# Performance work log

Measured on AMD Instinct MI355X. Metric: run time of the kernel, lower is better.

## Reference

```python
import jax, jax.numpy as jnp
import numpy as np

B, L, DIN, DM, NL = 2, 1024, 512, 1024, 4
E, N, R, K = 2048, 16, 64, 4  # d_inner, d_state, dt_rank, d_conv


def setup_inputs() -> dict:
    key = jax.random.key(0)
    ks = iter(jax.random.split(key, 32))
    rn = lambda sh, s=1.0: jax.random.normal(next(ks), sh, jnp.float32) * s
    A_init = jnp.broadcast_to(jnp.arange(1, N + 1, dtype=jnp.float32), (NL, E, N))
    return dict(
        x=rn((B, L, DIN)),
        z=rn((B, L, DIN)),
        ip_w=rn((DM, DIN), 0.02), ip_b=jnp.zeros((DM,), jnp.float32),
        ln_w=jnp.ones((NL, DM), jnp.float32), ln_b=jnp.zeros((NL, DM), jnp.float32),
        inproj_w=rn((NL, 2 * E, DM), 0.02),
        conv_w=rn((NL, E, K), 0.1), conv_b=jnp.zeros((NL, E), jnp.float32),
        xproj_w=rn((NL, R + 2 * N, E), 0.02),
        dtproj_w=rn((NL, E, R), 0.05), dtproj_b=rn((NL, E), 0.1),
        A_log=jnp.log(A_init),
        Dp=jnp.ones((NL, E), jnp.float32),
        outproj_w=rn((NL, DM, E), 0.02),
        fnorm_w=jnp.ones((DM,), jnp.float32), fnorm_b=jnp.zeros((DM,), jnp.float32),
        op_w=rn((DIN, DM), 0.02), op_b=jnp.zeros((DIN,), jnp.float32),
    )


def layernorm(x, w, b, eps=1e-5):
    m = x.mean(-1, keepdims=True)
    v = ((x - m) ** 2).mean(-1, keepdims=True)
    return (x - m) * jax.lax.rsqrt(v + eps) * w + b


def dwconv_causal(xm, w, b):
    # xm: (B, L, E); w: (E, K) depthwise kernel; causal left padding
    xc = xm.transpose(0, 2, 1)  # (B, E, L)
    out = jax.lax.conv_general_dilated(
        xc, w[:, None, :], (1,), [(K - 1, 0)],
        feature_group_count=E, dimension_numbers=('NCH', 'OIH', 'NCH'))
    return (out + b[:, None]).transpose(0, 2, 1)


def selective_scan(u, dt, A, Bm, Cm, D):
    # u, dt: (B, L, E); A: (E, N); Bm, Cm: (B, L, N); D: (E,)
    h0 = jnp.zeros((u.shape[0], E, N), u.dtype)

    def step(h, inp):
        dt_t, u_t, B_t, C_t = inp  # (B,E),(B,E),(B,N),(B,N)
        dA = jnp.exp(dt_t[..., None] * A)                      # (B, E, N)
        h = dA * h + (dt_t * u_t)[..., None] * B_t[:, None, :]  # (B, E, N)
        y = jnp.einsum('ben,bn->be', h, C_t)
        return h, y

    _, ys = jax.lax.scan(step, h0, (dt.transpose(1, 0, 2), u.transpose(1, 0, 2),
                                    Bm.transpose(1, 0, 2), Cm.transpose(1, 0, 2)))
    return ys.transpose(1, 0, 2) + u * D  # (B, L, E)


def mamba_block(x, inproj_w, conv_w, conv_b, xproj_w, dtproj_w, dtproj_b, A_log, Dp, outproj_w):
    xz = jnp.einsum('bld,ed->ble', x, inproj_w)  # (B, L, 2E)
    xm, zg = xz[..., :E], xz[..., E:]
    xm = jax.nn.silu(dwconv_causal(xm, conv_w, conv_b))
    x_dbl = jnp.einsum('ble,re->blr', xm, xproj_w)  # (B, L, R+2N)
    dt = jax.nn.softplus(jnp.einsum('blr,er->ble', x_dbl[..., :R], dtproj_w) + dtproj_b)
    Bm = x_dbl[..., R:R + N]
    Cm = x_dbl[..., R + N:]
    A = -jnp.exp(A_log)  # (E, N)
    y = selective_scan(xm, dt, A, Bm, Cm, Dp)
    y = y * jax.nn.silu(zg)
    return jnp.einsum('ble,de->bld', y, outproj_w)


def reference(x, z, ip_w, ip_b, ln_w, ln_b, inproj_w, conv_w, conv_b, xproj_w,
              dtproj_w, dtproj_b, A_log, Dp, outproj_w, fnorm_w, fnorm_b, op_w, op_b):
    # z is accepted but unused, matching the original forward(x, z)
    h = jnp.einsum('bld,hd->blh', x, ip_w) + ip_b
    for l in range(NL):
        hn = layernorm(h, ln_w[l], ln_b[l])
        h = h + mamba_block(hn, inproj_w[l], conv_w[l], conv_b[l], xproj_w[l],
                            dtproj_w[l], dtproj_b[l], A_log[l], Dp[l], outproj_w[l])
    h = layernorm(h, fnorm_w, fnorm_b)
    return jnp.einsum('blh,oh->blo', h, op_w) + op_b
```

## Files before the change

kernel.cpp:

```cpp
#include <hip/hip_runtime.h>
#include <math.h>

#define BB 2
#define LL 1024
#define DIN_ 512
#define DM_ 1024
#define NL_ 4
#define EE 2048
#define NN 16
#define RR 64
#define KK 4

#define NC 32
#define CT 32

typedef unsigned short ushort_t;
typedef unsigned int uint_t;

using frag_ab = __attribute__((ext_vector_type(8))) short;
using frag_cd = __attribute__((ext_vector_type(4))) float;

__device__ __forceinline__ float softplus_f(float x) {
    return fmaxf(x, 0.f) + log1pf(expf(-fabsf(x)));
}
__device__ __forceinline__ float silu_fast(float x) {
    return x / (1.f + __expf(-x));
}
__device__ __forceinline__ float bf2f(ushort_t x) {
    return __uint_as_float((uint_t)x << 16);
}
__device__ __forceinline__ ushort_t f2bf(float x) {
    uint_t u = __float_as_uint(x);
    uint_t r = (u + 0x7fffu + ((u >> 16) & 1u)) >> 16;
    return (ushort_t)r;
}
__device__ __forceinline__ void gload_lds16(const void* g, void* l) {
    __builtin_amdgcn_global_load_lds(
        (const __attribute__((address_space(1))) void*)g,
        (__attribute__((address_space(3))) void*)l, 16, 0, 0);
}

__global__ __launch_bounds__(256) void cvt_bf16_kernel(
    ushort_t* __restrict__ o, const float* __restrict__ in, int n4)
{
    int i = blockIdx.x * 256 + threadIdx.x;
    if (i >= n4) return;
    float4 v = ((const float4*)in)[i];
    ushort4 u;
    u.x = f2bf(v.x); u.y = f2bf(v.y); u.z = f2bf(v.z); u.w = f2bf(v.w);
    ((ushort4*)o)[i] = u;
}

template <int EPI, int NT, int OUTBF>
__global__ __launch_bounds__(256) void mgemm_kernel(
    void* __restrict__ Cp, const ushort_t* __restrict__ A,
    const ushort_t* __restrict__ W, const float* __restrict__ bias,
    int N, int K, int lda, int ldw, int ldc, int pstride)
{
    __shared__ __attribute__((aligned(16))) ushort_t As[2][8 * 512];
    __shared__ __attribute__((aligned(16))) ushort_t Bs[2][NT * 512];

    const int tid = threadIdx.x;
    const int w = tid >> 6;
    const int lane = tid & 63;
    const int r = lane & 15;
    const int q = lane >> 4;
    const int m0 = blockIdx.y * 128;
    const int n0 = blockIdx.x * (NT * 16);
    const int wm = w >> 1;
    const int wn = w & 1;
    const int NWT = NT / 2;

    frag_cd acc[4][NWT];
#pragma unroll
    for (int i = 0; i < 4; i++)
#pragma unroll
        for (int j = 0; j < NWT; j++)
#pragma unroll
            for (int t = 0; t < 4; t++) acc[i][j][t] = 0.f;

    size_t koff = (EPI == 5) ? (size_t)blockIdx.z * K : 0;
    const ushort_t* Ab = A + (size_t)m0 * lda + koff;
    const ushort_t* Wb = W + (size_t)n0 * ldw + koff;

    const int NFRAG = 8 + NT;
    auto stage = [&](int k0, int buf) {
        for (int F = w; F < NFRAG; F += 4) {
            if (F < 8) {
                gload_lds16(Ab + (size_t)(F * 16 + r) * lda + k0 + q * 8,
                            &As[buf][F * 512]);
            } else {
                int nt = F - 8;
                if (n0 + nt * 16 + r < N)
                    gload_lds16(Wb + (size_t)(nt * 16 + r) * ldw + k0 + q * 8,
                                &Bs[buf][nt * 512]);
            }
        }
    };

    stage(0, 0);
    int buf = 0;
    for (int k0 = 0; k0 < K; k0 += 32) {
        __syncthreads();
        if (k0 + 32 < K) stage(k0 + 32, buf ^ 1);
        frag_ab af[4], bf[NWT];
#pragma unroll
        for (int i = 0; i < 4; i++)
            af[i] = *(const frag_ab*)(&As[buf][(wm * 4 + i) * 512] + lane * 8);
#pragma unroll
        for (int j = 0; j < NWT; j++)
            bf[j] = *(const frag_ab*)(&Bs[buf][(wn * NWT + j) * 512] + lane * 8);
#pragma unroll
        for (int i = 0; i < 4; i++)
#pragma unroll
            for (int j = 0; j < NWT; j++)
                acc[i][j] = __builtin_amdgcn_mfma_f32_16x16x32_bf16(
                    af[i], bf[j], acc[i][j], 0, 0, 0);
        buf ^= 1;
    }

    float* Cf = (float*)Cp;
    ushort_t* Cb = (ushort_t*)Cp;
    float* Cpart = (EPI == 5) ? Cf + (size_t)blockIdx.z * pstride : Cf;
#pragma unroll
    for (int i = 0; i < 4; i++) {
        int mrow = m0 + (wm * 4 + i) * 16 + q * 4;
#pragma unroll
        for (int j = 0; j < NWT; j++) {
            int col = n0 + (wn * NWT + j) * 16 + r;
            if (col >= N) continue;
            float bv = (EPI == 2) ? bias[col] : 0.f;
#pragma unroll
            for (int t = 0; t < 4; t++) {
                float v = acc[i][j][t];
                size_t idx = (size_t)(mrow + t) * ldc + col;
                if (EPI == 5) { Cpart[idx] = v; continue; }
                if (EPI == 2) v = softplus_f(v + bv);
                if (OUTBF) Cb[idx] = f2bf(v);
                else       Cf[idx] = v;
            }
        }
    }
}

__global__ __launch_bounds__(256) void reduce_ln_kernel(
    float* __restrict__ h, ushort_t* __restrict__ hn,
    const float* __restrict__ parts, int nparts, int pstride4,
    const float* __restrict__ bias,
    const float* __restrict__ w, const float* __restrict__ b, int hasres)
{
    const int row = blockIdx.x;
    const int tid = threadIdx.x;
    const int i4 = row * (DM_ / 4) + tid;

    float4 v = make_float4(0.f, 0.f, 0.f, 0.f);
    if (hasres) v = ((const float4*)h)[i4];
    for (int p = 0; p < nparts; p++) {
        float4 t = ((const float4*)parts)[(size_t)p * pstride4 + i4];
        v.x += t.x; v.y += t.y; v.z += t.z; v.w += t.w;
    }
    if (bias) {
        float4 t = ((const float4*)bias)[tid];
        v.x += t.x; v.y += t.y; v.z += t.z; v.w += t.w;
    }
    ((float4*)h)[i4] = v;

    float s = v.x + v.y + v.z + v.w;
    float sq = v.x * v.x + v.y * v.y + v.z * v.z + v.w * v.w;
#pragma unroll
    for (int off = 32; off; off >>= 1) {
        s += __shfl_down(s, off);
        sq += __shfl_down(sq, off);
    }
    __shared__ float ls[4], lq[4];
    int wid = tid >> 6;
    if ((tid & 63) == 0) { ls[wid] = s; lq[wid] = sq; }
    __syncthreads();
    float S = ls[0] + ls[1] + ls[2] + ls[3];
    float Q = lq[0] + lq[1] + lq[2] + lq[3];
    float mean = S * (1.f / DM_);
    float var = Q * (1.f / DM_) - mean * mean;
    float inv = rsqrtf(var + 1e-5f);
    float4 wv = ((const float4*)w)[tid];
    float4 bv = ((const float4*)b)[tid];
    ushort4 o;
    o.x = f2bf((v.x - mean) * inv * wv.x + bv.x);
    o.y = f2bf((v.y - mean) * inv * wv.y + bv.y);
    o.z = f2bf((v.z - mean) * inv * wv.z + bv.z);
    o.w = f2bf((v.w - mean) * inv * wv.w + bv.w);
    ((ushort4*)hn)[i4] = o;
}

__global__ __launch_bounds__(256) void reduce_xdb_kernel(
    float* __restrict__ xdb, ushort_t* __restrict__ xdbb,
    const float* __restrict__ parts, int pstride4, int total4)
{
    int i = blockIdx.x * 256 + threadIdx.x;
    if (i >= total4) return;
    float4 v = make_float4(0.f, 0.f, 0.f, 0.f);
#pragma unroll
    for (int p = 0; p < 16; p++) {
        float4 t = ((const float4*)parts)[(size_t)p * pstride4 + i];
        v.x += t.x; v.y += t.y; v.z += t.z; v.w += t.w;
    }
    ((float4*)xdb)[i] = v;
    ushort4 u;
    u.x = f2bf(v.x); u.y = f2bf(v.y); u.z = f2bf(v.z); u.w = f2bf(v.w);
    ((ushort4*)xdbb)[i] = u;
}

__global__ __launch_bounds__(256) void reduce_bias_kernel(
    float* __restrict__ out, const float* __restrict__ parts,
    const float* __restrict__ bias, int pstride4, int n4, int total4)
{
    int i = blockIdx.x * 256 + threadIdx.x;
    if (i >= total4) return;
    float4 v = ((const float4*)bias)[i % n4];
#pragma unroll
    for (int p = 0; p < 4; p++) {
        float4 t = ((const float4*)parts)[(size_t)p * pstride4 + i];
        v.x += t.x; v.y += t.y; v.z += t.z; v.w += t.w;
    }
    ((float4*)out)[i] = v;
}

__global__ __launch_bounds__(256) void conv_silu_kernel(
    ushort_t* __restrict__ xm, const ushort_t* __restrict__ xz,
    const float* __restrict__ cw, const float* __restrict__ cb)
{
    const int e = blockIdx.x * 256 + threadIdx.x;
    const int t0 = blockIdx.y * 4;
    const int b = blockIdx.z;
    const ushort_t* X = xz + (size_t)b * LL * 2 * EE + e;
    float4 w4 = ((const float4*)cw)[e];
    float wk[4] = {w4.x, w4.y, w4.z, w4.w};
    float cbv = cb[e];
    float v[7];
#pragma unroll
    for (int k = 0; k < 7; k++) {
        int t = t0 - 3 + k;
        v[k] = (t >= 0) ? bf2f(X[(size_t)t * 2 * EE]) : 0.f;
    }
    ushort_t* Y = xm + ((size_t)b * LL + t0) * EE + e;
#pragma unroll
    for (int j = 0; j < 4; j++) {
        float acc = cbv;
#pragma unroll
        for (int k = 0; k < 4; k++) acc = fmaf(wk[k], v[j + k], acc);
        Y[(size_t)j * EE] = f2bf(silu_fast(acc));
    }
}

__global__ __launch_bounds__(256) void scan_phase1_kernel(
    float* __restrict__ Pg, float* __restrict__ Sg,
    const float* __restrict__ dt, const ushort_t* __restrict__ u,
    const float* __restrict__ xdb, const float* __restrict__ A_log)
{
    const int tid = threadIdx.x;
    const int e = blockIdx.x * 256 + tid;
    const int c = blockIdx.y;
    const int b = blockIdx.z;
    const int t0 = c * CT;

    __shared__ float Bs[CT][16];
    {
        int tt = tid >> 3;
        int jj = tid & 7;
        if (jj < 4) {
            float4 v = *(const float4*)(xdb + ((size_t)(b * LL + t0 + tt) * 96 + 64 + jj * 4));
            *(float4*)&Bs[tt][jj * 4] = v;
        }
    }
    __syncthreads();

    float Ae[16];
#pragma unroll
    for (int k = 0; k < 4; k++) {
        float4 a = *(const float4*)(A_log + (size_t)e * NN + k * 4);
        Ae[k * 4 + 0] = -__expf(a.x);
        Ae[k * 4 + 1] = -__expf(a.y);
        Ae[k * 4 + 2] = -__expf(a.z);
        Ae[k * 4 + 3] = -__expf(a.w);
    }

    float S[16];
#pragma unroll
    for (int n = 0; n < 16; n++) S[n] = 0.f;
    float Dsum = 0.f;

    const float* dt_p = dt + (size_t)(b * LL + t0) * EE + e;
    const ushort_t* u_p = u + (size_t)(b * LL + t0) * EE + e;

    float dtv = dt_p[0];
    float uv = bf2f(u_p[0]);
#pragma unroll 4
    for (int i = 0; i < CT; i++) {
        int ip = (i + 1 < CT) ? i + 1 : i;
        float dtn = dt_p[(size_t)ip * EE];
        float un = bf2f(u_p[(size_t)ip * EE]);
        float dtu = dtv * uv;
        Dsum += dtv;
        float Bv[16];
#pragma unroll
        for (int k = 0; k < 4; k++)
            *(float4*)&Bv[k * 4] = *(const float4*)&Bs[i][k * 4];
#pragma unroll
        for (int n = 0; n < 16; n++) {
            float da = __expf(dtv * Ae[n]);
            S[n] = fmaf(da, S[n], dtu * Bv[n]);
        }
        dtv = dtn; uv = un;
    }

    size_t o = ((size_t)(b * NC + c) * EE + e) * 16;
#pragma unroll
    for (int k = 0; k < 4; k++) {
        float4 p4;
        p4.x = __expf(Dsum * Ae[k * 4 + 0]);
        p4.y = __expf(Dsum * Ae[k * 4 + 1]);
        p4.z = __expf(Dsum * Ae[k * 4 + 2]);
        p4.w = __expf(Dsum * Ae[k * 4 + 3]);
        *(float4*)(Pg + o + k * 4) = p4;
        *(float4*)(Sg + o + k * 4) = *(float4*)&S[k * 4];
    }
}

__global__ __launch_bounds__(256) void scan_combine_kernel(
    float* __restrict__ Pg, const float* __restrict__ Sg)
{
    const int f = blockIdx.x * 256 + threadIdx.x;
    const int b = blockIdx.y;
    float h = 0.f;
    for (int c = 0; c < NC; c++) {
        size_t o = (size_t)(b * NC + c) * EE * 16 + f;
        float p = Pg[o];
        float s = Sg[o];
        h = fmaf(p, h, s);
        Pg[o] = h;
    }
}

__global__ __launch_bounds__(256) void scan_phase2_kernel(
    ushort_t* __restrict__ y, const float* __restrict__ Pg,
    const float* __restrict__ dt, const ushort_t* __restrict__ u,
    const float* __restrict__ xdb, const ushort_t* __restrict__ xz,
    const float* __restrict__ A_log, const float* __restrict__ Dp)
{
    const int tid = threadIdx.x;
    const int e = blockIdx.x * 256 + tid;
    const int c = blockIdx.y;
    const int b = blockIdx.z;
    const int t0 = c * CT;

    __shared__ float Bs[CT][16], Cs[CT][16];
    {
        int tt = tid >> 3;
        int jj = tid & 7;
        float4 v = *(const float4*)(xdb + ((size_t)(b * LL + t0 + tt) * 96 + 64 + jj * 4));
        if (jj < 4) *(float4*)&Bs[tt][jj * 4] = v;
        else        *(float4*)&Cs[tt][(jj - 4) * 4] = v;
    }
    __syncthreads();

    float Ae[16];
#pragma unroll
    for (int k = 0; k < 4; k++) {
        float4 a = *(const float4*)(A_log + (size_t)e * NN + k * 4);
        Ae[k * 4 + 0] = -__expf(a.x);
        Ae[k * 4 + 1] = -__expf(a.y);
        Ae[k * 4 + 2] = -__expf(a.z);
        Ae[k * 4 + 3] = -__expf(a.w);
    }

    float h[16];
    if (c == 0) {
#pragma unroll
        for (int n = 0; n < 16; n++) h[n] = 0.f;
    } else {
        size_t o = ((size_t)(b * NC + (c - 1)) * EE + e) * 16;
#pragma unroll
        for (int k = 0; k < 4; k++)
            *(float4*)&h[k * 4] = *(const float4*)(Pg + o + k * 4);
    }

    const float Dv = Dp[e];
    const float* dt_p = dt + (size_t)(b * LL + t0) * EE + e;
    const ushort_t* u_p = u + (size_t)(b * LL + t0) * EE + e;
    const ushort_t* zg_p = xz + (size_t)(b * LL + t0) * 2 * EE + EE + e;
    ushort_t* y_p = y + (size_t)(b * LL + t0) * EE + e;

    float dtv = dt_p[0];
    float uv = bf2f(u_p[0]);
    float zv = bf2f(zg_p[0]);
#pragma unroll 4
    for (int i = 0; i < CT; i++) {
        int ip = (i + 1 < CT) ? i + 1 : i;
        float dtn = dt_p[(size_t)ip * EE];
        float un = bf2f(u_p[(size_t)ip * EE]);
        float zn = bf2f(zg_p[(size_t)ip * 2 * EE]);
        float dtu = dtv * uv;
        float Bv[16], Cv[16];
#pragma unroll
        for (int k = 0; k < 4; k++) {
            *(float4*)&Bv[k * 4] = *(const float4*)&Bs[i][k * 4];
            *(float4*)&Cv[k * 4] = *(const float4*)&Cs[i][k * 4];
        }
        float yv = 0.f;
#pragma unroll
        for (int n = 0; n < 16; n++) {
            float da = __expf(dtv * Ae[n]);
            h[n] = fmaf(da, h[n], dtu * Bv[n]);
            yv = fmaf(h[n], Cv[n], yv);
        }
        y_p[(size_t)i * EE] = f2bf((yv + uv * Dv) * silu_fast(zv));
        dtv = dtn; uv = un; zv = zn;
    }
}

extern "C" void kernel_launch(void* const* d_in, const int* in_sizes, int n_in,
                              void* d_out, int out_size, void* d_ws, size_t ws_size,
                              hipStream_t stream)
{
    const float* x = (const float*)d_in[0];
    const float* ip_w = (const float*)d_in[2];
    const float* ip_b = (const float*)d_in[3];
    const float* ln_w = (const float*)d_in[4];
    const float* ln_b = (const float*)d_in[5];
    const float* inproj_w = (const float*)d_in[6];
    const float* conv_w = (const float*)d_in[7];
    const float* conv_b = (const float*)d_in[8];
    const float* xproj_w = (const float*)d_in[9];
    const float* dtproj_w = (const float*)d_in[10];
    const float* dtproj_b = (const float*)d_in[11];
    const float* A_log = (const float*)d_in[12];
    const float* Dp = (const float*)d_in[13];
    const float* outproj_w = (const float*)d_in[14];
    const float* fnorm_w = (const float*)d_in[15];
    const float* fnorm_b = (const float*)d_in[16];
    const float* op_w = (const float*)d_in[17];
    const float* op_b = (const float*)d_in[18];
    float* out = (float*)d_out;

    const size_t BL = (size_t)BB * LL;

    float* fp = (float*)d_ws;
    float* h = fp;           fp += BL * DM_;
    float* xdb = fp;         fp += BL * 96;
    float* dtb = fp;         fp += BL * EE;
    float* Pg = fp;          fp += (size_t)BB * NC * EE * 16;
    float* Sg = fp;          fp += (size_t)BB * NC * EE * 16;
    float* parts = dtb;
    ushort_t* us = (ushort_t*)fp;
    ushort_t* xb = us;       us += BL * DIN_;
    ushort_t* hnb = us;      us += BL * DM_;
    ushort_t* xzb = us;      us += BL * 2 * EE;
    ushort_t* xm = us;       us += BL * EE;
    ushort_t* xdbb = us;     us += BL * 96;
    ushort_t* yb = us;       us += BL * EE;
    ushort_t* ipwb = us;     us += (size_t)DM_ * DIN_;
    ushort_t* inprojb = us;  us += (size_t)NL_ * 2 * EE * DM_;
    ushort_t* xprojb = us;   us += (size_t)NL_ * 96 * EE;
    ushort_t* dtprojb = us;  us += (size_t)NL_ * EE * RR;
    ushort_t* outprojb = us; us += (size_t)NL_ * DM_ * EE;
    ushort_t* opwb = us;     us += (size_t)DIN_ * DM_;

    dim3 blk(256);
    auto cvt = [&](ushort_t* dst, const float* src, size_t n) {
        int n4 = (int)(n / 4);
        cvt_bf16_kernel<<<dim3((n4 + 255) / 256), blk, 0, stream>>>(dst, src, n4);
    };

    cvt(xb, x, BL * DIN_);
    cvt(ipwb, ip_w, (size_t)DM_ * DIN_);
    cvt(inprojb, inproj_w, (size_t)NL_ * 2 * EE * DM_);
    cvt(xprojb, xproj_w, (size_t)NL_ * 96 * EE);
    cvt(dtprojb, dtproj_w, (size_t)NL_ * EE * RR);
    cvt(outprojb, outproj_w, (size_t)NL_ * DM_ * EE);
    cvt(opwb, op_w, (size_t)DIN_ * DM_);

    const int PS_DM = (int)(BL * DM_);

    mgemm_kernel<5, 4, 0><<<dim3(DM_ / 64, BL / 128, 2), blk, 0, stream>>>(
        parts, xb, ipwb, nullptr, DM_, DIN_ / 2, DIN_, DIN_, DM_, PS_DM);
    reduce_ln_kernel<<<dim3(BL), blk, 0, stream>>>(
        h, hnb, parts, 2, PS_DM / 4, ip_b, ln_w, ln_b, 0);

    for (int l = 0; l < NL_; l++) {
        mgemm_kernel<0, 8, 1><<<dim3(2 * EE / 128, BL / 128), blk, 0, stream>>>(
            xzb, hnb, inprojb + (size_t)l * 2 * EE * DM_, nullptr,
            2 * EE, DM_, DM_, DM_, 2 * EE, 0);
        conv_silu_kernel<<<dim3(EE / 256, LL / 4, BB), blk, 0, stream>>>(
            xm, xzb, conv_w + l * EE * KK, conv_b + l * EE);
        mgemm_kernel<5, 8, 0><<<dim3(1, BL / 128, 16), blk, 0, stream>>>(
            parts, xm, xprojb + (size_t)l * 96 * EE, nullptr,
            96, EE / 16, EE, EE, 96, (int)(BL * 96));
        reduce_xdb_kernel<<<dim3((int)(BL * 96 / 4 + 255) / 256), blk, 0, stream>>>(
            xdb, xdbb, parts, (int)(BL * 96 / 4), (int)(BL * 96 / 4));
        mgemm_kernel<2, 8, 0><<<dim3(EE / 128, BL / 128), blk, 0, stream>>>(
            dtb, xdbb, dtprojb + (size_t)l * EE * RR, dtproj_b + l * EE,
            EE, RR, 96, RR, EE, 0);

        scan_phase1_kernel<<<dim3(EE / 256, NC, BB), blk, 0, stream>>>(
            Pg, Sg, dtb, xm, xdb, A_log + (size_t)l * EE * NN);
        scan_combine_kernel<<<dim3(EE * 16 / 256, BB), blk, 0, stream>>>(Pg, Sg);
        scan_phase2_kernel<<<dim3(EE / 256, NC, BB), blk, 0, stream>>>(
            yb, Pg, dtb, xm, xdb, xzb, A_log + (size_t)l * EE * NN, Dp + l * EE);

        mgemm_kernel<5, 8, 0><<<dim3(DM_ / 128, BL / 128, 4), blk, 0, stream>>>(
            parts, yb, outprojb + (size_t)l * DM_ * EE, nullptr,
            DM_, EE / 4, EE, EE, DM_, PS_DM);
        const float* nw = (l + 1 < NL_) ? ln_w + (l + 1) * DM_ : fnorm_w;
        const float* nb = (l + 1 < NL_) ? ln_b + (l + 1) * DM_ : fnorm_b;
        reduce_ln_kernel<<<dim3(BL), blk, 0, stream>>>(
            h, hnb, parts, 4, PS_DM / 4, nullptr, nw, nb, 1);
    }

    mgemm_kernel<5, 4, 0><<<dim3(DIN_ / 64, BL / 128, 4), blk, 0, stream>>>(
        parts, hnb, opwb, nullptr, DIN_, DM_ / 4, DM_, DM_, DIN_, (int)(BL * DIN_));
    reduce_bias_kernel<<<dim3((int)(BL * DIN_ / 4 + 255) / 256), blk, 0, stream>>>(
        out, parts, op_b, (int)(BL * DIN_ / 4), DIN_ / 4, (int)(BL * DIN_ / 4));
}
```

Before: 917.9 us.

## Fuse bf16 conversions, deepen GEMM K-tile to 64, batch scan-combine loads

Merges the seven separate fp32-to-bf16 conversion launches into one kernel that picks its source segment from a cumulative offset table. Doubles the GEMM K step to 64 with precomputed per-thread global pointers, halving the barrier and stage count per K at the cost of twice the LDS per stage. Also changes the chunk-combine scan to load all chunk prefixes into registers before the serial recurrence, so the loads are independent instead of serialised.

```diff
diff --git a/kernel.cpp b/kernel.cpp
--- a/kernel.cpp
+++ b/kernel.cpp
@@ -40,15 +40,24 @@
         (__attribute__((address_space(3))) void*)l, 16, 0, 0);
 }
 
-__global__ __launch_bounds__(256) void cvt_bf16_kernel(
-    ushort_t* __restrict__ o, const float* __restrict__ in, int n4)
+struct CvtArgs {
+    const float* src[7];
+    ushort_t* dst[7];
+    int cum[8];
+};
+
+__global__ __launch_bounds__(256) void cvt_all_kernel(CvtArgs a)
 {
     int i = blockIdx.x * 256 + threadIdx.x;
-    if (i >= n4) return;
-    float4 v = ((const float4*)in)[i];
+    if (i >= a.cum[7]) return;
+    int s = 0;
+#pragma unroll
+    for (int k = 1; k < 7; k++) s += (i >= a.cum[k]) ? 1 : 0;
+    int j = i - a.cum[s];
+    float4 v = ((const float4*)a.src[s])[j];
     ushort4 u;
     u.x = f2bf(v.x); u.y = f2bf(v.y); u.z = f2bf(v.z); u.w = f2bf(v.w);
-    ((ushort4*)o)[i] = u;
+    ((ushort4*)a.dst[s])[j] = u;
 }
 
 template <int EPI, int NT, int OUTBF>
@@ -57,8 +66,7 @@
     const ushort_t* __restrict__ W, const float* __restrict__ bias,
     int N, int K, int lda, int ldw, int ldc, int pstride)
 {
-    __shared__ __attribute__((aligned(16))) ushort_t As[2][8 * 512];
-    __shared__ __attribute__((aligned(16))) ushort_t Bs[2][NT * 512];
+    __shared__ __attribute__((aligned(16))) ushort_t smem[2][(8 + NT) * 1024];
 
     const int tid = threadIdx.x;
     const int w = tid >> 6;
@@ -83,39 +91,54 @@
     const ushort_t* Ab = A + (size_t)m0 * lda + koff;
     const ushort_t* Wb = W + (size_t)n0 * ldw + koff;
 
-    const int NFRAG = 8 + NT;
-    auto stage = [&](int k0, int buf) {
-        for (int F = w; F < NFRAG; F += 4) {
-            if (F < 8) {
-                gload_lds16(Ab + (size_t)(F * 16 + r) * lda + k0 + q * 8,
-                            &As[buf][F * 512]);
-            } else {
-                int nt = F - 8;
-                if (n0 + nt * 16 + r < N)
-                    gload_lds16(Wb + (size_t)(nt * 16 + r) * ldw + k0 + q * 8,
-                                &Bs[buf][nt * 512]);
-            }
+    constexpr int FPW = (8 + NT) * 2 / 4;
+    const ushort_t* gp[FPW];
+    bool ok[FPW];
+#pragma unroll
+    for (int fi = 0; fi < FPW; fi++) {
+        int F = w + fi * 4;
+        int kk = F & 1;
+        int G = F >> 1;
+        if (G < 8) {
+            gp[fi] = Ab + (size_t)(G * 16 + r) * lda + kk * 32 + q * 8;
+            ok[fi] = true;
+        } else {
+            int nt = G - 8;
+            ok[fi] = (n0 + nt * 16 + r) < N;
+            gp[fi] = Wb + (size_t)(nt * 16 + r) * ldw + kk * 32 + q * 8;
+        }
+    }
+
+    auto stage = [&](int buf) {
+#pragma unroll
+        for (int fi = 0; fi < FPW; fi++) {
+            if (ok[fi])
+                gload_lds16(gp[fi], &smem[buf][(w + fi * 4) * 512]);
+            gp[fi] += 64;
         }
     };
 
-    stage(0, 0);
+    stage(0);
     int buf = 0;
-    for (int k0 = 0; k0 < K; k0 += 32) {
+    for (int k0 = 0; k0 < K; k0 += 64) {
         __syncthreads();
-        if (k0 + 32 < K) stage(k0 + 32, buf ^ 1);
-        frag_ab af[4], bf[NWT];
-#pragma unroll
-        for (int i = 0; i < 4; i++)
-            af[i] = *(const frag_ab*)(&As[buf][(wm * 4 + i) * 512] + lane * 8);
-#pragma unroll
-        for (int j = 0; j < NWT; j++)
-            bf[j] = *(const frag_ab*)(&Bs[buf][(wn * NWT + j) * 512] + lane * 8);
-#pragma unroll
-        for (int i = 0; i < 4; i++)
+        if (k0 + 64 < K) stage(buf ^ 1);
+#pragma unroll
+        for (int kk = 0; kk < 2; kk++) {
+            frag_ab af[4], bf[NWT];
+#pragma unroll
+            for (int i = 0; i < 4; i++)
+                af[i] = *(const frag_ab*)(&smem[buf][((wm * 4 + i) * 2 + kk) * 512] + lane * 8);
 #pragma unroll
             for (int j = 0; j < NWT; j++)
-                acc[i][j] = __builtin_amdgcn_mfma_f32_16x16x32_bf16(
-                    af[i], bf[j], acc[i][j], 0, 0, 0);
+                bf[j] = *(const frag_ab*)(&smem[buf][((8 + wn * NWT + j) * 2 + kk) * 512] + lane * 8);
+#pragma unroll
+            for (int i = 0; i < 4; i++)
+#pragma unroll
+                for (int j = 0; j < NWT; j++)
+                    acc[i][j] = __builtin_amdgcn_mfma_f32_16x16x32_bf16(
+                        af[i], bf[j], acc[i][j], 0, 0, 0);
+        }
         buf ^= 1;
     }
 
@@ -330,14 +353,24 @@
 {
     const int f = blockIdx.x * 256 + threadIdx.x;
     const int b = blockIdx.y;
+    const size_t stride = (size_t)EE * 16;
+    const size_t base = (size_t)b * NC * stride + f;
+
+    float P[NC], S[NC];
+#pragma unroll
+    for (int c = 0; c < NC; c++) {
+        P[c] = Pg[base + c * stride];
+        S[c] = Sg[base + c * stride];
+    }
     float h = 0.f;
+#pragma unroll
     for (int c = 0; c < NC; c++) {
-        size_t o = (size_t)(b * NC + c) * EE * 16 + f;
-        float p = Pg[o];
-        float s = Sg[o];
-        h = fmaf(p, h, s);
-        Pg[o] = h;
-    }
+        h = fmaf(P[c], h, S[c]);
+        P[c] = h;
+    }
+#pragma unroll
+    for (int c = 0; c < NC; c++)
+        Pg[base + c * stride] = P[c];
 }
 
 __global__ __launch_bounds__(256) void scan_phase2_kernel(
@@ -465,18 +498,24 @@
     ushort_t* opwb = us;     us += (size_t)DIN_ * DM_;
 
     dim3 blk(256);
-    auto cvt = [&](ushort_t* dst, const float* src, size_t n) {
-        int n4 = (int)(n / 4);
-        cvt_bf16_kernel<<<dim3((n4 + 255) / 256), blk, 0, stream>>>(dst, src, n4);
-    };
-
-    cvt(xb, x, BL * DIN_);
-    cvt(ipwb, ip_w, (size_t)DM_ * DIN_);
-    cvt(inprojb, inproj_w, (size_t)NL_ * 2 * EE * DM_);
-    cvt(xprojb, xproj_w, (size_t)NL_ * 96 * EE);
-    cvt(dtprojb, dtproj_w, (size_t)NL_ * EE * RR);
-    cvt(outprojb, outproj_w, (size_t)NL_ * DM_ * EE);
-    cvt(opwb, op_w, (size_t)DIN_ * DM_);
+
+    {
+        CvtArgs a;
+        const float* srcs[7] = {x, ip_w, inproj_w, xproj_w, dtproj_w, outproj_w, op_w};
+        ushort_t* dsts[7] = {xb, ipwb, inprojb, xprojb, dtprojb, outprojb, opwb};
+        size_t ns[7] = {BL * DIN_, (size_t)DM_ * DIN_, (size_t)NL_ * 2 * EE * DM_,
+                        (size_t)NL_ * 96 * EE, (size_t)NL_ * EE * RR,
+                        (size_t)NL_ * DM_ * EE, (size_t)DIN_ * DM_};
+        int cum = 0;
+        for (int s = 0; s < 7; s++) {
+            a.src[s] = srcs[s];
+            a.dst[s] = dsts[s];
+            a.cum[s] = cum;
+            cum += (int)(ns[s] / 4);
+        }
+        a.cum[7] = cum;
+        cvt_all_kernel<<<dim3((cum + 255) / 256), blk, 0, stream>>>(a);
+    }
 
     const int PS_DM = (int)(BL * DM_);
 
```

New measurement: 895.5 us. 1.03x faster.
